# Performance work log

Measured on AMD Instinct MI355X. Metric: run time of the kernel, lower is better.

Reference implementation:

```python
import jax, jax.numpy as jnp
import numpy as np

EPS = 1e-8

def setup_inputs() -> dict:
    key = jax.random.key(0)
    k0, k1, k2, k3, k4 = jax.random.split(key, 5)
    B, N, K, Q, L, F = 8, 5, 5, 4, 128, 768
    support_emb = jax.random.normal(k0, (B, N, K, L, F), dtype=jnp.float32)
    query_emb = jax.random.normal(k1, (B, N * Q, L, F), dtype=jnp.float32)
    B_mask = jax.random.randint(k2, (B, N, K, L), 0, 2, dtype=jnp.int32)
    I_mask = jax.random.randint(k3, (B, N, K, L), 0, 2, dtype=jnp.int32)
    trigger_label = jax.random.randint(k4, (B, N * Q, L), 0, 2 * N + 1, dtype=jnp.int32)
    return {"support_emb": support_emb, "query_emb": query_emb, "B_mask": B_mask,
            "I_mask": I_mask, "trigger_label": trigger_label, "N": N, "K": K, "Q": Q}

def _proto(support_emb, Bm, Im, N):
    # support_emb: (B,N,K,L,F); Bm/Im: (B,N,K,L) float
    sum_B = jnp.einsum('bnklf,bnkl->bnf', support_emb, Bm)
    cnt_B = Bm.sum((2, 3))[..., None] + EPS
    pB = sum_B / cnt_B                                   # (B,N,F)
    sum_I = jnp.einsum('bnklf,bnkl->bnf', support_emb, Im)
    cnt_I = Im.sum((2, 3))[..., None] + EPS
    pI = sum_I / cnt_I                                   # (B,N,F)
    Om = 1.0 - Bm - Im                                   # (B,N,K,L)
    sum_O = jnp.einsum('bnklf,bnkl->bf', support_emb, Om)
    cnt_O = Om.sum((1, 2, 3))[:, None] + EPS
    pO = sum_O / cnt_O                                   # (B,F)
    Bsz, F = pO.shape
    # interleave: tags [O, B_0, I_0, B_1, I_1, ...]
    pBI = jnp.stack([pB, pI], axis=2).reshape(Bsz, 2 * N, F)
    return jnp.concatenate([pO[:, None, :], pBI], axis=1)  # (B, 2N+1, F)

def reference(support_emb, query_emb, B_mask, I_mask, trigger_label, N, K, Q):
    dt = support_emb.dtype
    Bm = B_mask.astype(dt)
    Im = I_mask.astype(dt)
    prototype = _proto(support_emb, Bm, Im, N)             # (B, 2N+1, F)
    # similarity: broadcast dot product -> batched GEMM
    logits = jnp.einsum('bqlf,btf->bqlt', query_emb, prototype)  # (B, NQ, L, 2N+1)
    T = logits.shape[-1]
    flat = logits.reshape(-1, T)
    pred = jnp.argmax(flat, axis=1)
    lab = trigger_label.reshape(-1)
    logp = jax.nn.log_softmax(flat, axis=-1)
    loss = -jnp.take_along_axis(logp, lab[:, None], axis=1).mean()
    return (loss, logits, pred)
```

## Files before the change

kernel.cpp:

```cpp
#include <hip/hip_runtime.h>
#include <cstdint>
#include <cstddef>

#define EPS 1e-8f

#define Bsz 8
#define Nn  5
#define Kk  5
#define Ll  128
#define Ff  768
#define Tt  11
#define KL  640
#define ROWS_PER_B 2560
#define NROWS 20480
#define F4  192
#define BN  40

#define S1_ROWS 16
#define S1_CH   (KL / S1_ROWS)
#define S1_NBLK (BN * S1_CH)
#define PART_STRIDE (3 * Ff)
#define PART_STRIDE4 (PART_STRIDE / 4)

typedef float v2f __attribute__((ext_vector_type(2)));

__global__ __launch_bounds__(192) void stage1(
    const float* __restrict__ sup,
    const int*   __restrict__ Bm,
    const int*   __restrict__ Im,
    float* __restrict__ part,
    float* __restrict__ pcnt)
{
    int blk = blockIdx.x;
    int bn  = blk / S1_CH;
    int ch  = blk - bn * S1_CH;
    int tid = threadIdx.x;

    const float4* sp = (const float4*)(sup + ((size_t)bn * KL + ch * S1_ROWS) * Ff) + tid;
    const int*    bp = Bm + bn * KL + ch * S1_ROWS;
    const int*    ip = Im + bn * KL + ch * S1_ROWS;

    v2f tB0 = {0.f,0.f}, tB1 = tB0, tI0 = tB0, tI1 = tB0, tA0 = tB0, tA1 = tB0;
    int cB = 0, cI = 0;

    #pragma unroll
    for (int h = 0; h < 2; ++h) {
        float4 v[8];
        #pragma unroll
        for (int j = 0; j < 8; ++j) v[j] = sp[(h * 8 + j) * F4];
        #pragma unroll
        for (int j = 0; j < 8; ++j) {
            int p = h * 8 + j;
            v2f lo = {v[j].x, v[j].y};
            v2f hi = {v[j].z, v[j].w};
            tA0 += lo; tA1 += hi;
            if (bp[p]) { tB0 += lo; tB1 += hi; ++cB; }
            if (ip[p]) { tI0 += lo; tI1 += hi; ++cI; }
        }
    }

    float4* o = (float4*)(part + (size_t)blk * PART_STRIDE);
    float4 rB = {tB0.x, tB0.y, tB1.x, tB1.y};
    float4 rI = {tI0.x, tI0.y, tI1.x, tI1.y};
    float4 rA = {tA0.x, tA0.y, tA1.x, tA1.y};
    o[tid]          = rB;
    o[F4 + tid]     = rI;
    o[2 * F4 + tid] = rA;

    if (tid == 0) {
        pcnt[2 * (size_t)blk]     = (float)cB;
        pcnt[2 * (size_t)blk + 1] = (float)cI;
    }
}

__global__ __launch_bounds__(768) void stage2(
    const float* __restrict__ part,
    const float* __restrict__ pcnt,
    float* __restrict__ bnsum,
    float* __restrict__ cnt,
    float* __restrict__ loss_out)
{
    __shared__ float4 red[768];

    int blk = blockIdx.x;
    int bn  = blk / 3;
    int set = blk - bn * 3;
    int tid = threadIdx.x;

    if (blk == 0 && tid == 0) loss_out[0] = 0.0f;

    int q  = tid / F4;
    int f4 = tid - q * F4;

    const float4* src = (const float4*)part + ((size_t)bn * 3 * S1_CH + set) * F4 + f4;
    float4 s = {0, 0, 0, 0};
    float4 v[10];
    #pragma unroll
    for (int k = 0; k < 10; ++k) v[k] = src[(size_t)(q * 10 + k) * PART_STRIDE4];
    #pragma unroll
    for (int k = 0; k < 10; ++k) {
        s.x += v[k].x; s.y += v[k].y; s.z += v[k].z; s.w += v[k].w;
    }
    red[tid] = s;

    if (set < 2 && tid < 64) {
        float cv = (tid < S1_CH) ? pcnt[2 * ((size_t)bn * S1_CH + tid) + set] : 0.0f;
        #pragma unroll
        for (int off = 32; off > 0; off >>= 1) cv += __shfl_xor(cv, off, 64);
        if (tid == 0) cnt[2 * bn + set] = cv;
    }

    __syncthreads();
    if (q == 0) {
        float4 a = red[f4];
        float4 b = red[F4 + f4];
        float4 c = red[2 * F4 + f4];
        float4 d = red[3 * F4 + f4];
        float4 t4 = {a.x + b.x + c.x + d.x, a.y + b.y + c.y + d.y,
                     a.z + b.z + c.z + d.z, a.w + b.w + c.w + d.w};
        ((float4*)bnsum)[((size_t)bn * 3 + set) * F4 + f4] = t4;
    }
}

__global__ __launch_bounds__(192) void stage2b(
    const float* __restrict__ bnsum,
    const float* __restrict__ cnt,
    float* __restrict__ proto)
{
    int b  = blockIdx.x / Tt;
    int t  = blockIdx.x - b * Tt;
    int f4 = threadIdx.x;

    const float4* bs = (const float4*)bnsum + (size_t)b * Nn * 3 * F4;

    float scale;
    if (t == 0) {
        float cO = (float)(KL * Nn);
        #pragma unroll
        for (int k = 0; k < 2 * Nn; ++k) cO -= cnt[2 * Nn * b + k];
        scale = 1.0f / (cO + EPS);
    } else {
        scale = 1.0f / (cnt[2 * Nn * b + (t - 1)] + EPS);
    }

    float4 val;
    if (t == 0) {
        float sx = 0, sy = 0, sz = 0, sw = 0;
        #pragma unroll
        for (int n = 0; n < Nn; ++n) {
            float4 A  = bs[(n * 3 + 2) * F4 + f4];
            float4 Bv = bs[(n * 3 + 0) * F4 + f4];
            float4 Iv = bs[(n * 3 + 1) * F4 + f4];
            sx += A.x - Bv.x - Iv.x; sy += A.y - Bv.y - Iv.y;
            sz += A.z - Bv.z - Iv.z; sw += A.w - Bv.w - Iv.w;
        }
        val.x = sx; val.y = sy; val.z = sz; val.w = sw;
    } else {
        int n  = (t - 1) >> 1;
        int st = (t - 1) & 1;
        val = bs[(n * 3 + st) * F4 + f4];
    }
    val.x *= scale; val.y *= scale; val.z *= scale; val.w *= scale;
    ((float4*)proto)[((size_t)b * Tt + t) * F4 + f4] = val;
}

#define S3_ROWS 32
#define S3_NBLK (NROWS / S3_ROWS)
#define S3_BPB  (ROWS_PER_B / S3_ROWS)

#define DOT_STEP(JV, UU, WW)                                              \
    {                                                                     \
        _Pragma("unroll")                                                 \
        for (int t = 0; t < Tt; ++t) {                                    \
            float4 pv = pb[t * F4 + (JV) * 16];                           \
            float d0 = a0[t], d1 = a1[t];                                 \
            d0 = fmaf((UU).x, pv.x, d0); d0 = fmaf((UU).y, pv.y, d0);     \
            d0 = fmaf((UU).z, pv.z, d0); d0 = fmaf((UU).w, pv.w, d0);     \
            d1 = fmaf((WW).x, pv.x, d1); d1 = fmaf((WW).y, pv.y, d1);     \
            d1 = fmaf((WW).z, pv.z, d1); d1 = fmaf((WW).w, pv.w, d1);     \
            a0[t] = d0; a1[t] = d1;                                       \
        }                                                                 \
    }

__global__ __launch_bounds__(256, 3) void stage3(
    const float* __restrict__ query,
    const float* __restrict__ proto,
    const int*   __restrict__ label,
    float* __restrict__ out_logits,
    float* __restrict__ out_pred,
    float* __restrict__ loss_out)
{
    __shared__ float4 ldsP[Tt * F4];

    int blk = blockIdx.x;
    int b   = blk / S3_BPB;
    int tid = threadIdx.x;

    const float4* pp = (const float4*)proto + (size_t)b * Tt * F4;
    for (int idx = tid; idx < Tt * F4; idx += 256) ldsP[idx] = pp[idx];
    __syncthreads();

    int p = tid >> 4;
    int s = tid & 15;

    size_t row0 = (size_t)blk * S3_ROWS + p * 2;
    const float4* q0 = (const float4*)query + row0 * F4 + s;
    const float4* q1 = q0 + F4;

    float a0[Tt], a1[Tt];
    #pragma unroll
    for (int t = 0; t < Tt; ++t) { a0[t] = 0.0f; a1[t] = 0.0f; }

    float4 u0[6], w0[6], u1[6], w1[6];
    #pragma unroll
    for (int j = 0; j < 6; ++j) { u0[j] = q0[j * 16]; w0[j] = q1[j * 16]; }
    #pragma unroll
    for (int j = 0; j < 6; ++j) { u1[j] = q0[(j + 6) * 16]; w1[j] = q1[(j + 6) * 16]; }

    const float4* pb = ldsP + s;
    #pragma unroll
    for (int j = 0; j < 6; ++j) DOT_STEP(j, u0[j], w0[j]);
    #pragma unroll
    for (int j = 0; j < 6; ++j) DOT_STEP(j + 6, u1[j], w1[j]);

    #pragma unroll
    for (int t = 0; t < Tt; ++t) {
        a0[t] += __shfl_xor(a0[t], 1, 16); a0[t] += __shfl_xor(a0[t], 2, 16);
        a0[t] += __shfl_xor(a0[t], 4, 16); a0[t] += __shfl_xor(a0[t], 8, 16);
        a1[t] += __shfl_xor(a1[t], 1, 16); a1[t] += __shfl_xor(a1[t], 2, 16);
        a1[t] += __shfl_xor(a1[t], 4, 16); a1[t] += __shfl_xor(a1[t], 8, 16);
    }

    float wloss = 0.0f;
    if (s < 2) {
        float rv[Tt];
        #pragma unroll
        for (int t = 0; t < Tt; ++t) rv[t] = s ? a1[t] : a0[t];
        size_t grow = row0 + s;

        float m = rv[0]; int bt = 0;
        #pragma unroll
        for (int t = 1; t < Tt; ++t) if (rv[t] > m) { m = rv[t]; bt = t; }
        float sum = 0.0f;
        #pragma unroll
        for (int t = 0; t < Tt; ++t) sum += __expf(rv[t] - m);
        int lab = label[grow];
        float labv = rv[0];
        #pragma unroll
        for (int t = 1; t < Tt; ++t) labv = (lab == t) ? rv[t] : labv;
        #pragma unroll
        for (int t = 0; t < Tt; ++t) out_logits[grow * Tt + t] = rv[t];
        out_pred[grow] = (float)bt;
        wloss = (m + __logf(sum)) - labv;
    }
    #pragma unroll
    for (int off = 32; off > 0; off >>= 1) wloss += __shfl_xor(wloss, off, 64);
    if ((tid & 63) == 0) atomicAdd(loss_out, wloss * (1.0f / (float)NROWS));
}

extern "C" void kernel_launch(void* const* d_in, const int* in_sizes, int n_in,
                              void* d_out, int out_size, void* d_ws, size_t ws_size,
                              hipStream_t stream) {
    const float* sup   = (const float*)d_in[0];
    const float* query = (const float*)d_in[1];
    const int*   Bm    = (const int*)d_in[2];
    const int*   Im    = (const int*)d_in[3];
    const int*   lab   = (const int*)d_in[4];

    float* w     = (float*)d_ws;
    float* part  = w;
    float* pcnt  = part + (size_t)S1_NBLK * PART_STRIDE;
    float* bnsum = pcnt + 2 * S1_NBLK;
    float* cnt   = bnsum + (size_t)BN * 3 * Ff;
    float* proto = cnt + 2 * BN;

    float* loss_out   = (float*)d_out;
    float* out_logits = (float*)d_out + 1;
    float* out_pred   = (float*)d_out + 1 + (size_t)NROWS * Tt;

    stage1<<<S1_NBLK, 192, 0, stream>>>(sup, Bm, Im, part, pcnt);
    stage2<<<3 * BN, 768, 0, stream>>>(part, pcnt, bnsum, cnt, loss_out);
    stage2b<<<Bsz * Tt, 192, 0, stream>>>(bnsum, cnt, proto);
    stage3<<<S3_NBLK, 256, 0, stream>>>(query, proto, lab,
                                        out_logits, out_pred, loss_out);
}
```

Measured before the change: 217.9 us.

## Enlarge stage tiles, simplify partial reduction, register-block 4 query rows

Stage1 now reduces 64 rows per block instead of 16, which cuts the number of partial sums stage2 has to combine. Stage2 becomes a flat one-thread-per-output reduction with no shared memory. Stage3 computes 4 query rows per 16-lane group, so each LDS prototype read feeds four dot products, and it prefetches the next query slice one step ahead. The loss is reduced within the block first, so there is one atomic per block instead of one per wavefront. Costs: fewer stage1 blocks (400) lowers parallelism for the streaming reduction, stage3 uses more registers, and the explicit occupancy hint is dropped.

New measurement: 195.5 us. -10.3%, faster.

```diff
diff --git a/kernel.cpp b/kernel.cpp
--- a/kernel.cpp
+++ b/kernel.cpp
@@ -16,7 +16,7 @@
 #define F4  192
 #define BN  40
 
-#define S1_ROWS 16
+#define S1_ROWS 64
 #define S1_CH   (KL / S1_ROWS)
 #define S1_NBLK (BN * S1_CH)
 #define PART_STRIDE (3 * Ff)
@@ -43,11 +43,10 @@
     v2f tB0 = {0.f,0.f}, tB1 = tB0, tI0 = tB0, tI1 = tB0, tA0 = tB0, tA1 = tB0;
     int cB = 0, cI = 0;
 
-    #pragma unroll
-    for (int h = 0; h < 2; ++h) {
+    for (int h = 0; h < S1_ROWS / 8; ++h) {
         float4 v[8];
         #pragma unroll
-        for (int j = 0; j < 8; ++j) v[j] = sp[(h * 8 + j) * F4];
+        for (int j = 0; j < 8; ++j) v[j] = sp[(size_t)(h * 8 + j) * F4];
         #pragma unroll
         for (int j = 0; j < 8; ++j) {
             int p = h * 8 + j;
@@ -73,52 +72,39 @@
     }
 }
 
-__global__ __launch_bounds__(768) void stage2(
+__global__ __launch_bounds__(256) void stage2(
     const float* __restrict__ part,
     const float* __restrict__ pcnt,
     float* __restrict__ bnsum,
     float* __restrict__ cnt,
     float* __restrict__ loss_out)
 {
-    __shared__ float4 red[768];
-
-    int blk = blockIdx.x;
-    int bn  = blk / 3;
-    int set = blk - bn * 3;
-    int tid = threadIdx.x;
-
-    if (blk == 0 && tid == 0) loss_out[0] = 0.0f;
-
-    int q  = tid / F4;
-    int f4 = tid - q * F4;
-
-    const float4* src = (const float4*)part + ((size_t)bn * 3 * S1_CH + set) * F4 + f4;
+    int gid = blockIdx.x * 256 + threadIdx.x;
+    if (gid == 0) loss_out[0] = 0.0f;
+
+    int bn  = gid / (3 * F4);
+    int r   = gid - bn * (3 * F4);
+    int set = r / F4;
+    int f4  = r - set * F4;
+
+    const float4* src = (const float4*)part + ((size_t)bn * S1_CH * 3 + set) * F4 + f4;
     float4 s = {0, 0, 0, 0};
-    float4 v[10];
-    #pragma unroll
-    for (int k = 0; k < 10; ++k) v[k] = src[(size_t)(q * 10 + k) * PART_STRIDE4];
-    #pragma unroll
-    for (int k = 0; k < 10; ++k) {
-        s.x += v[k].x; s.y += v[k].y; s.z += v[k].z; s.w += v[k].w;
-    }
-    red[tid] = s;
-
-    if (set < 2 && tid < 64) {
-        float cv = (tid < S1_CH) ? pcnt[2 * ((size_t)bn * S1_CH + tid) + set] : 0.0f;
-        #pragma unroll
-        for (int off = 32; off > 0; off >>= 1) cv += __shfl_xor(cv, off, 64);
-        if (tid == 0) cnt[2 * bn + set] = cv;
-    }
-
-    __syncthreads();
-    if (q == 0) {
-        float4 a = red[f4];
-        float4 b = red[F4 + f4];
-        float4 c = red[2 * F4 + f4];
-        float4 d = red[3 * F4 + f4];
-        float4 t4 = {a.x + b.x + c.x + d.x, a.y + b.y + c.y + d.y,
-                     a.z + b.z + c.z + d.z, a.w + b.w + c.w + d.w};
-        ((float4*)bnsum)[((size_t)bn * 3 + set) * F4 + f4] = t4;
+    float4 v[S1_CH];
+    #pragma unroll
+    for (int c = 0; c < S1_CH; ++c) v[c] = src[(size_t)c * PART_STRIDE4];
+    #pragma unroll
+    for (int c = 0; c < S1_CH; ++c) {
+        s.x += v[c].x; s.y += v[c].y; s.z += v[c].z; s.w += v[c].w;
+    }
+    ((float4*)bnsum)[((size_t)bn * 3 + set) * F4 + f4] = s;
+
+    if (gid < 2 * BN) {
+        int bn2  = gid >> 1;
+        int set2 = gid & 1;
+        float cv = 0.0f;
+        #pragma unroll
+        for (int c = 0; c < S1_CH; ++c) cv += pcnt[2 * ((size_t)bn2 * S1_CH + c) + set2];
+        cnt[gid] = cv;
     }
 }
 
@@ -164,25 +150,10 @@
     ((float4*)proto)[((size_t)b * Tt + t) * F4 + f4] = val;
 }
 
-#define S3_ROWS 32
+#define S3_ROWS 64
 #define S3_NBLK (NROWS / S3_ROWS)
-#define S3_BPB  (ROWS_PER_B / S3_ROWS)
-
-#define DOT_STEP(JV, UU, WW)                                              \
-    {                                                                     \
-        _Pragma("unroll")                                                 \
-        for (int t = 0; t < Tt; ++t) {                                    \
-            float4 pv = pb[t * F4 + (JV) * 16];                           \
-            float d0 = a0[t], d1 = a1[t];                                 \
-            d0 = fmaf((UU).x, pv.x, d0); d0 = fmaf((UU).y, pv.y, d0);     \
-            d0 = fmaf((UU).z, pv.z, d0); d0 = fmaf((UU).w, pv.w, d0);     \
-            d1 = fmaf((WW).x, pv.x, d1); d1 = fmaf((WW).y, pv.y, d1);     \
-            d1 = fmaf((WW).z, pv.z, d1); d1 = fmaf((WW).w, pv.w, d1);     \
-            a0[t] = d0; a1[t] = d1;                                       \
-        }                                                                 \
-    }
-
-__global__ __launch_bounds__(256, 3) void stage3(
+
+__global__ __launch_bounds__(256) void stage3(
     const float* __restrict__ query,
     const float* __restrict__ proto,
     const int*   __restrict__ label,
@@ -191,10 +162,11 @@
     float* __restrict__ loss_out)
 {
     __shared__ float4 ldsP[Tt * F4];
+    __shared__ float  lred[4];
 
     int blk = blockIdx.x;
-    int b   = blk / S3_BPB;
     int tid = threadIdx.x;
+    int b   = blk / (ROWS_PER_B / S3_ROWS);
 
     const float4* pp = (const float4*)proto + (size_t)b * Tt * F4;
     for (int idx = tid; idx < Tt * F4; idx += 256) ldsP[idx] = pp[idx];
@@ -203,25 +175,40 @@
     int p = tid >> 4;
     int s = tid & 15;
 
-    size_t row0 = (size_t)blk * S3_ROWS + p * 2;
-    const float4* q0 = (const float4*)query + row0 * F4 + s;
-    const float4* q1 = q0 + F4;
-
-    float a0[Tt], a1[Tt];
-    #pragma unroll
-    for (int t = 0; t < Tt; ++t) { a0[t] = 0.0f; a1[t] = 0.0f; }
-
-    float4 u0[6], w0[6], u1[6], w1[6];
-    #pragma unroll
-    for (int j = 0; j < 6; ++j) { u0[j] = q0[j * 16]; w0[j] = q1[j * 16]; }
-    #pragma unroll
-    for (int j = 0; j < 6; ++j) { u1[j] = q0[(j + 6) * 16]; w1[j] = q1[(j + 6) * 16]; }
+    size_t row0 = (size_t)blk * S3_ROWS + p * 4;
+    const float4* qb = (const float4*)query + row0 * F4 + s;
+
+    float a0[Tt], a1[Tt], a2[Tt], a3[Tt];
+    #pragma unroll
+    for (int t = 0; t < Tt; ++t) { a0[t] = 0.f; a1[t] = 0.f; a2[t] = 0.f; a3[t] = 0.f; }
+
+    float4 u0 = qb[0 * F4], u1 = qb[1 * F4], u2 = qb[2 * F4], u3 = qb[3 * F4];
 
     const float4* pb = ldsP + s;
     #pragma unroll
-    for (int j = 0; j < 6; ++j) DOT_STEP(j, u0[j], w0[j]);
-    #pragma unroll
-    for (int j = 0; j < 6; ++j) DOT_STEP(j + 6, u1[j], w1[j]);
+    for (int j = 0; j < 12; ++j) {
+        float4 w0, w1, w2, w3;
+        if (j < 11) {
+            int o = (j + 1) * 16;
+            w0 = qb[0 * F4 + o]; w1 = qb[1 * F4 + o];
+            w2 = qb[2 * F4 + o]; w3 = qb[3 * F4 + o];
+        }
+        #pragma unroll
+        for (int t = 0; t < Tt; ++t) {
+            float4 pv = pb[t * F4 + j * 16];
+            float d0 = a0[t], d1 = a1[t], d2 = a2[t], d3 = a3[t];
+            d0 = fmaf(u0.x, pv.x, d0); d0 = fmaf(u0.y, pv.y, d0);
+            d0 = fmaf(u0.z, pv.z, d0); d0 = fmaf(u0.w, pv.w, d0);
+            d1 = fmaf(u1.x, pv.x, d1); d1 = fmaf(u1.y, pv.y, d1);
+            d1 = fmaf(u1.z, pv.z, d1); d1 = fmaf(u1.w, pv.w, d1);
+            d2 = fmaf(u2.x, pv.x, d2); d2 = fmaf(u2.y, pv.y, d2);
+            d2 = fmaf(u2.z, pv.z, d2); d2 = fmaf(u2.w, pv.w, d2);
+            d3 = fmaf(u3.x, pv.x, d3); d3 = fmaf(u3.y, pv.y, d3);
+            d3 = fmaf(u3.z, pv.z, d3); d3 = fmaf(u3.w, pv.w, d3);
+            a0[t] = d0; a1[t] = d1; a2[t] = d2; a3[t] = d3;
+        }
+        if (j < 11) { u0 = w0; u1 = w1; u2 = w2; u3 = w3; }
+    }
 
     #pragma unroll
     for (int t = 0; t < Tt; ++t) {
@@ -229,13 +216,18 @@
         a0[t] += __shfl_xor(a0[t], 4, 16); a0[t] += __shfl_xor(a0[t], 8, 16);
         a1[t] += __shfl_xor(a1[t], 1, 16); a1[t] += __shfl_xor(a1[t], 2, 16);
         a1[t] += __shfl_xor(a1[t], 4, 16); a1[t] += __shfl_xor(a1[t], 8, 16);
+        a2[t] += __shfl_xor(a2[t], 1, 16); a2[t] += __shfl_xor(a2[t], 2, 16);
+        a2[t] += __shfl_xor(a2[t], 4, 16); a2[t] += __shfl_xor(a2[t], 8, 16);
+        a3[t] += __shfl_xor(a3[t], 1, 16); a3[t] += __shfl_xor(a3[t], 2, 16);
+        a3[t] += __shfl_xor(a3[t], 4, 16); a3[t] += __shfl_xor(a3[t], 8, 16);
     }
 
     float wloss = 0.0f;
-    if (s < 2) {
+    if (s < 4) {
         float rv[Tt];
         #pragma unroll
-        for (int t = 0; t < Tt; ++t) rv[t] = s ? a1[t] : a0[t];
+        for (int t = 0; t < Tt; ++t)
+            rv[t] = (s == 0) ? a0[t] : (s == 1) ? a1[t] : (s == 2) ? a2[t] : a3[t];
         size_t grow = row0 + s;
 
         float m = rv[0]; int bt = 0;
@@ -255,7 +247,10 @@
     }
     #pragma unroll
     for (int off = 32; off > 0; off >>= 1) wloss += __shfl_xor(wloss, off, 64);
-    if ((tid & 63) == 0) atomicAdd(loss_out, wloss * (1.0f / (float)NROWS));
+    if ((tid & 63) == 0) lred[tid >> 6] = wloss;
+    __syncthreads();
+    if (tid == 0)
+        atomicAdd(loss_out, (lred[0] + lred[1] + lred[2] + lred[3]) * (1.0f / (float)NROWS));
 }
 
 extern "C" void kernel_launch(void* const* d_in, const int* in_sizes, int n_in,
@@ -279,7 +274,7 @@
     float* out_pred   = (float*)d_out + 1 + (size_t)NROWS * Tt;
 
     stage1<<<S1_NBLK, 192, 0, stream>>>(sup, Bm, Im, part, pcnt);
-    stage2<<<3 * BN, 768, 0, stream>>>(part, pcnt, bnsum, cnt, loss_out);
+    stage2<<<90, 256, 0, stream>>>(part, pcnt, bnsum, cnt, loss_out);
     stage2b<<<Bsz * Tt, 192, 0, stream>>>(bnsum, cnt, proto);
     stage3<<<S3_NBLK, 256, 0, stream>>>(query, proto, lab,
                                         out_logits, out_pred, loss_out);
```
